# Performance work log

Hardware: AMD Instinct MI355X
Metric: run time of the kernel (lower is better)

Reference implementation:

```python
import jax, jax.numpy as jnp
import numpy as np

TEMPERATURE = 0.5
EPS = 1e-8  # torch CosineSimilarity eps


def setup_inputs() -> dict:
    key = jax.random.key(0)
    k1, k2 = jax.random.split(key)
    zis = jax.random.normal(k1, (65536, 256), dtype=jnp.float32)
    zjs = jax.random.normal(k2, (65536, 256), dtype=jnp.float32)
    # default soft labels: one-hot on the positive (first) logit column
    soft_labels = jnp.zeros((4, 3), dtype=jnp.float32).at[:, 0].set(1.0)
    return {"zis": zis, "zjs": zjs, "soft_labels": soft_labels}


def reference(zis, zjs, soft_labels):
    n, d = zis.shape
    nc = n // 2  # number of chunks of size 2
    zi = zis.reshape(nc, 2, d)
    zj = zjs.reshape(nc, 2, d)
    reps = jnp.concatenate([zj, zi], axis=1)  # (nc, 4, d) = cat([zjs, zis])
    # cosine similarity with eps clamp as in torch.nn.CosineSimilarity
    norm = jnp.maximum(jnp.linalg.norm(reps, axis=-1, keepdims=True), EPS)
    reps_n = reps / norm
    sim = jnp.einsum('nid,njd->nij', reps_n, reps_n)  # (nc, 4, 4)
    # positives: diag(sim, +2) then diag(sim, -2) -> cols [2,3,0,1]
    pos = sim[:, jnp.arange(4), jnp.array([2, 3, 0, 1])]  # (nc, 4)
    # negatives: mask removes main diag and +-2 diagonals -> 2 cols per row
    neg_idx = jnp.array([[1, 3], [0, 2], [1, 3], [0, 2]])  # (4, 2)
    neg = jnp.take_along_axis(sim, neg_idx[None, :, :], axis=2)  # (nc, 4, 2)
    logits = jnp.concatenate([pos[..., None], neg], axis=-1) / TEMPERATURE  # (nc,4,3)
    # criterion: exp-normalize (softmax) then -(log ps * soft_labels).sum()
    logp = jax.nn.log_softmax(logits, axis=-1)
    loss = -(logp * soft_labels[None, :, :]).sum()
    return loss / (2 * n)
```

## Files before the change

kernel.cpp:

```cpp
#include <hip/hip_runtime.h>
#include <math.h>


constexpr int D = 256;

__device__ __forceinline__ float dot4(float4 a, float4 b) {
    return a.x * b.x + a.y * b.y + a.z * b.z + a.w * b.w;
}

__device__ __forceinline__ float wred(float x) {
#pragma unroll
    for (int off = 1; off < 64; off <<= 1) x += __shfl_xor(x, off, 64);
    return x;
}

__device__ __forceinline__ float rowloss(float a, float b, float c,
                                         float s0, float s1, float s2) {
    float m = fmaxf(fmaxf(a, b), c);
    float lse = m + logf(expf(a - m) + expf(b - m) + expf(c - m));
    return s0 * (lse - a) + s1 * (lse - b) + s2 * (lse - c);
}

__global__ __launch_bounds__(256) void ntxent_stage1(
    const float* __restrict__ zis, const float* __restrict__ zjs,
    const float* __restrict__ sl, float* __restrict__ partial, int nc) {
    const int lane = threadIdx.x & 63;
    const int wid  = threadIdx.x >> 6;
    const int wpb  = blockDim.x >> 6;
    const int gw   = blockIdx.x * wpb + wid;
    const int nw   = gridDim.x * wpb;

    const float sl00 = sl[0],  sl01 = sl[1],  sl02 = sl[2];
    const float sl10 = sl[3],  sl11 = sl[4],  sl12 = sl[5];
    const float sl20 = sl[6],  sl21 = sl[7],  sl22 = sl[8];
    const float sl30 = sl[9],  sl31 = sl[10], sl32 = sl[11];

    float wsum = 0.0f;
    for (int g = gw; g < nc; g += nw) {
        const float4* r0 = (const float4*)(zjs + (size_t)(2 * g) * D);
        const float4* r1 = (const float4*)(zjs + (size_t)(2 * g + 1) * D);
        const float4* r2 = (const float4*)(zis + (size_t)(2 * g) * D);
        const float4* r3 = (const float4*)(zis + (size_t)(2 * g + 1) * D);
        float4 v0 = r0[lane];
        float4 v1 = r1[lane];
        float4 v2 = r2[lane];
        float4 v3 = r3[lane];

        float n0 = dot4(v0, v0), n1 = dot4(v1, v1);
        float n2 = dot4(v2, v2), n3 = dot4(v3, v3);
        float d01 = dot4(v0, v1), d02 = dot4(v0, v2), d03 = dot4(v0, v3);
        float d12 = dot4(v1, v2), d13 = dot4(v1, v3), d23 = dot4(v2, v3);

        n0 = wred(n0);  n1 = wred(n1);  n2 = wred(n2);  n3 = wred(n3);
        d01 = wred(d01); d02 = wred(d02); d03 = wred(d03);
        d12 = wred(d12); d13 = wred(d13); d23 = wred(d23);

        const float i0 = 1.0f / fmaxf(sqrtf(n0), 1e-8f);
        const float i1 = 1.0f / fmaxf(sqrtf(n1), 1e-8f);
        const float i2 = 1.0f / fmaxf(sqrtf(n2), 1e-8f);
        const float i3 = 1.0f / fmaxf(sqrtf(n3), 1e-8f);

        const float s01 = 2.0f * d01 * i0 * i1;
        const float s02 = 2.0f * d02 * i0 * i2;
        const float s03 = 2.0f * d03 * i0 * i3;
        const float s12 = 2.0f * d12 * i1 * i2;
        const float s13 = 2.0f * d13 * i1 * i3;
        const float s23 = 2.0f * d23 * i2 * i3;

        float gl = 0.0f;
        gl += rowloss(s02, s01, s03, sl00, sl01, sl02);
        gl += rowloss(s13, s01, s12, sl10, sl11, sl12);
        gl += rowloss(s02, s12, s23, sl20, sl21, sl22);
        gl += rowloss(s13, s03, s23, sl30, sl31, sl32);
        wsum += gl;
    }

    __shared__ float smem[8];
    if (lane == 0) smem[wid] = wsum;
    __syncthreads();
    if (threadIdx.x == 0) {
        float b = 0.0f;
        for (int i = 0; i < wpb; ++i) b += smem[i];
        partial[blockIdx.x] = b;
    }
}

__global__ __launch_bounds__(256) void ntxent_stage2(
    const float* __restrict__ partial, int nparts, double inv_div,
    float* __restrict__ out) {
    double acc = 0.0;
    for (int i = threadIdx.x; i < nparts; i += 256) acc += (double)partial[i];
#pragma unroll
    for (int off = 1; off < 64; off <<= 1) acc += __shfl_xor(acc, off, 64);
    __shared__ double sm[4];
    const int wid = threadIdx.x >> 6;
    if ((threadIdx.x & 63) == 0) sm[wid] = acc;
    __syncthreads();
    if (threadIdx.x == 0) {
        double t = sm[0] + sm[1] + sm[2] + sm[3];
        out[0] = (float)(t * inv_div);
    }
}

extern "C" void kernel_launch(void* const* d_in, const int* in_sizes, int n_in,
                              void* d_out, int out_size, void* d_ws, size_t ws_size,
                              hipStream_t stream) {
    const float* zis = (const float*)d_in[0];
    const float* zjs = (const float*)d_in[1];
    const float* sl  = (const float*)d_in[2];
    float* out = (float*)d_out;
    float* partial = (float*)d_ws;

    const int n  = in_sizes[0] / D;
    const int nc = n / 2;

    const int blocks = 2048;
    ntxent_stage1<<<blocks, 256, 0, stream>>>(zis, zjs, sl, partial, nc);

    const double inv_div = 1.0 / (2.0 * (double)n);
    ntxent_stage2<<<1, 256, 0, stream>>>(partial, blocks, inv_div, out);
}
```

Before: 151.1 us.

## Process four chunks per wave with 16-lane groups and shorter shuffle reductions

Each wave now splits into four 16-lane groups, and each group handles one chunk of four rows. Every lane loads four float4 per row and accumulates locally. This cuts the ten cross-lane reductions from six shuffle steps over 64 lanes to four steps over 16 lanes, and it gives each lane more loads in flight per iteration. The per-group results are scaled by 1/16, and a single full-wave reduction runs at the end. The cost is more registers per thread, and each group loads rows with a stride inside the wave rather than one contiguous row per wave.

```diff
diff --git a/kernel.cpp b/kernel.cpp
--- a/kernel.cpp
+++ b/kernel.cpp
@@ -5,12 +5,14 @@
 constexpr int D = 256;
 
 __device__ __forceinline__ float dot4(float4 a, float4 b) {
-    return a.x * b.x + a.y * b.y + a.z * b.z + a.w * b.w;
+    return fmaf(a.x, b.x, fmaf(a.y, b.y, fmaf(a.z, b.z, a.w * b.w)));
 }
 
-__device__ __forceinline__ float wred(float x) {
-#pragma unroll
-    for (int off = 1; off < 64; off <<= 1) x += __shfl_xor(x, off, 64);
+__device__ __forceinline__ float red16(float x) {
+    x += __shfl_xor(x, 1);
+    x += __shfl_xor(x, 2);
+    x += __shfl_xor(x, 4);
+    x += __shfl_xor(x, 8);
     return x;
 }
 
@@ -26,9 +28,12 @@
     const float* __restrict__ sl, float* __restrict__ partial, int nc) {
     const int lane = threadIdx.x & 63;
     const int wid  = threadIdx.x >> 6;
-    const int wpb  = blockDim.x >> 6;
-    const int gw   = blockIdx.x * wpb + wid;
-    const int nw   = gridDim.x * wpb;
+    const int t    = lane & 15;
+    const int q    = lane >> 4;
+
+    const int gwave = blockIdx.x * 4 + wid;
+    const int nwave = gridDim.x * 4;
+    const int nquad = (nc + 3) >> 2;
 
     const float sl00 = sl[0],  sl01 = sl[1],  sl02 = sl[2];
     const float sl10 = sl[3],  sl11 = sl[4],  sl12 = sl[5];
@@ -36,24 +41,38 @@
     const float sl30 = sl[9],  sl31 = sl[10], sl32 = sl[11];
 
     float wsum = 0.0f;
-    for (int g = gw; g < nc; g += nw) {
-        const float4* r0 = (const float4*)(zjs + (size_t)(2 * g) * D);
-        const float4* r1 = (const float4*)(zjs + (size_t)(2 * g + 1) * D);
-        const float4* r2 = (const float4*)(zis + (size_t)(2 * g) * D);
-        const float4* r3 = (const float4*)(zis + (size_t)(2 * g + 1) * D);
-        float4 v0 = r0[lane];
-        float4 v1 = r1[lane];
-        float4 v2 = r2[lane];
-        float4 v3 = r3[lane];
+    for (int quad = gwave; quad < nquad; quad += nwave) {
+        const int g = quad * 4 + q;
+        const bool valid = g < nc;
+        const int gc = valid ? g : 0;
 
-        float n0 = dot4(v0, v0), n1 = dot4(v1, v1);
-        float n2 = dot4(v2, v2), n3 = dot4(v3, v3);
-        float d01 = dot4(v0, v1), d02 = dot4(v0, v2), d03 = dot4(v0, v3);
-        float d12 = dot4(v1, v2), d13 = dot4(v1, v3), d23 = dot4(v2, v3);
+        const float* rj = zjs + (size_t)(2 * gc) * D;
+        const float* ri = zis + (size_t)(2 * gc) * D;
+        const int o = t * 4;
 
-        n0 = wred(n0);  n1 = wred(n1);  n2 = wred(n2);  n3 = wred(n3);
-        d01 = wred(d01); d02 = wred(d02); d03 = wred(d03);
-        d12 = wred(d12); d13 = wred(d13); d23 = wred(d23);
+        float4 v0[4], v1[4], v2[4], v3[4];
+#pragma unroll
+        for (int c = 0; c < 4; ++c) {
+            v0[c] = *(const float4*)(rj + c * 64 + o);
+            v1[c] = *(const float4*)(rj + D + c * 64 + o);
+            v2[c] = *(const float4*)(ri + c * 64 + o);
+            v3[c] = *(const float4*)(ri + D + c * 64 + o);
+        }
+
+        float n0 = 0, n1 = 0, n2 = 0, n3 = 0;
+        float d01 = 0, d02 = 0, d03 = 0, d12 = 0, d13 = 0, d23 = 0;
+#pragma unroll
+        for (int c = 0; c < 4; ++c) {
+            n0 += dot4(v0[c], v0[c]);  n1 += dot4(v1[c], v1[c]);
+            n2 += dot4(v2[c], v2[c]);  n3 += dot4(v3[c], v3[c]);
+            d01 += dot4(v0[c], v1[c]); d02 += dot4(v0[c], v2[c]);
+            d03 += dot4(v0[c], v3[c]); d12 += dot4(v1[c], v2[c]);
+            d13 += dot4(v1[c], v3[c]); d23 += dot4(v2[c], v3[c]);
+        }
+
+        n0 = red16(n0);  n1 = red16(n1);  n2 = red16(n2);  n3 = red16(n3);
+        d01 = red16(d01); d02 = red16(d02); d03 = red16(d03);
+        d12 = red16(d12); d13 = red16(d13); d23 = red16(d23);
 
         const float i0 = 1.0f / fmaxf(sqrtf(n0), 1e-8f);
         const float i1 = 1.0f / fmaxf(sqrtf(n1), 1e-8f);
@@ -72,17 +91,18 @@
         gl += rowloss(s13, s01, s12, sl10, sl11, sl12);
         gl += rowloss(s02, s12, s23, sl20, sl21, sl22);
         gl += rowloss(s13, s03, s23, sl30, sl31, sl32);
-        wsum += gl;
+        if (valid) wsum += gl;
     }
+    wsum *= 0.0625f;
 
-    __shared__ float smem[8];
+#pragma unroll
+    for (int off = 1; off < 64; off <<= 1) wsum += __shfl_xor(wsum, off);
+
+    __shared__ float smem[4];
     if (lane == 0) smem[wid] = wsum;
     __syncthreads();
-    if (threadIdx.x == 0) {
-        float b = 0.0f;
-        for (int i = 0; i < wpb; ++i) b += smem[i];
-        partial[blockIdx.x] = b;
-    }
+    if (threadIdx.x == 0)
+        partial[blockIdx.x] = smem[0] + smem[1] + smem[2] + smem[3];
 }
 
 __global__ __launch_bounds__(256) void ntxent_stage2(
@@ -91,15 +111,12 @@
     double acc = 0.0;
     for (int i = threadIdx.x; i < nparts; i += 256) acc += (double)partial[i];
 #pragma unroll
-    for (int off = 1; off < 64; off <<= 1) acc += __shfl_xor(acc, off, 64);
+    for (int off = 1; off < 64; off <<= 1) acc += __shfl_xor(acc, off);
     __shared__ double sm[4];
     const int wid = threadIdx.x >> 6;
     if ((threadIdx.x & 63) == 0) sm[wid] = acc;
     __syncthreads();
-    if (threadIdx.x == 0) {
-        double t = sm[0] + sm[1] + sm[2] + sm[3];
-        out[0] = (float)(t * inv_div);
-    }
+    if (threadIdx.x == 0) out[0] = (float)((sm[0] + sm[1] + sm[2] + sm[3]) * inv_div);
 }
 
 extern "C" void kernel_launch(void* const* d_in, const int* in_sizes, int n_in,
```

Result: no change. 148.6 us (-1.6%).
